# Optimization experiments

Measured on AMD Instinct MI355X. Metric: run time of the kernel, lower is better.

Reference implementation:

```python
import jax, jax.numpy as jnp
import numpy as np

B, N, C = 512, 512, 96  # N = D*H*W with D=H=W=8


def _conv3d(x, w, b, groups=1):
    # x: [B, C, D, H, W], w: [O, I/groups, kd, kh, kw]
    y = jax.lax.conv_general_dilated(
        x, w, window_strides=(1, 1, 1), padding='SAME',
        dimension_numbers=('NCDHW', 'OIDHW', 'NCDHW'),
        feature_group_count=groups)
    return y + b[None, :, None, None, None]


def setup_inputs() -> dict:
    key = jax.random.key(0)
    ks = jax.random.split(key, 8)
    s1 = 0.1   # keep pre-softmax logits in a sane range
    sd = 0.2
    inp = {
        'x': jax.random.normal(ks[0], (B, N, C), jnp.float32),
        'wq1': jax.random.normal(ks[1], (C, C, 1, 1, 1), jnp.float32) * s1,
        'bq1': jnp.zeros((C,), jnp.float32),
        'wk1': jax.random.normal(ks[2], (C, C, 1, 1, 1), jnp.float32) * s1,
        'bk1': jnp.zeros((C,), jnp.float32),
        'wv1': jax.random.normal(ks[3], (C, C, 1, 1, 1), jnp.float32) * s1,
        'bv1': jnp.zeros((C,), jnp.float32),
        'wqd': jax.random.normal(ks[4], (C, 1, 3, 3, 3), jnp.float32) * sd,
        'bqd': jnp.zeros((C,), jnp.float32),
        'wkd': jax.random.normal(ks[5], (C, 1, 3, 3, 3), jnp.float32) * sd,
        'bkd': jnp.zeros((C,), jnp.float32),
        'wvd': jax.random.normal(ks[6], (C, 1, 3, 3, 3), jnp.float32) * sd,
        'bvd': jnp.zeros((C,), jnp.float32),
    }
    return inp


def reference(x, wq1, bq1, wk1, bk1, wv1, bv1, wqd, bqd, wkd, bkd, wvd, bvd):
    b, n, c = x.shape
    d = int(round(n ** (1.0 / 3.0)))
    # [B, N, C] -> [B, C, D, H, W]
    x5 = x.reshape(b, d, d, d, c).transpose(0, 4, 1, 2, 3)
    q = _conv3d(_conv3d(x5, wq1, bq1), wqd, bqd, groups=c)
    k = _conv3d(_conv3d(x5, wk1, bk1), wkd, bkd, groups=c)
    v = _conv3d(_conv3d(x5, wv1, bv1), wvd, bvd, groups=c)
    # [B, C, D, H, W] -> [B, N, C]
    q = q.transpose(0, 2, 3, 4, 1).reshape(b, n, c)
    k = k.transpose(0, 2, 3, 4, 1).reshape(b, n, c)
    v = v.transpose(0, 2, 3, 4, 1).reshape(b, n, c)
    attn = jnp.einsum('bnc,bmc->bnm', q, k) / jnp.sqrt(jnp.float32(c))
    attn = jax.nn.softmax(attn, axis=-1)
    out = jnp.einsum('bnm,bmc->bnc', attn, v)
    return out
```

## Files before the change

### kernel.cpp

```cpp
#include <hip/hip_runtime.h>
#include <math.h>

typedef _Float16 f16;
typedef _Float16 f16x2 __attribute__((ext_vector_type(2)));
typedef _Float16 f16x8 __attribute__((ext_vector_type(8)));
typedef __fp16 fp16x2 __attribute__((ext_vector_type(2)));
typedef float f32x4 __attribute__((ext_vector_type(4)));

union F2U { f16x2 h; fp16x2 p; unsigned u; };
union U2H { uint2 q; f16x2 h[2]; f16 f[4]; };
union U4H { uint4 q; f16x2 h[4]; f16 f[8]; };

__device__ __forceinline__ f16x2 uAsH(unsigned u) { F2U c; c.u = u; return c.h; }
__device__ __forceinline__ unsigned hAsU(f16x2 h) { F2U c; c.h = h; return c.u; }
__device__ __forceinline__ unsigned pAsU(fp16x2 p) { F2U c; c.p = p; return c.u; }

constexpr size_t PL = (size_t)512 * 512 * 96;

__global__ __launch_bounds__(1024, 4) void k12_fused(
    const float* __restrict__ x,
    const float* __restrict__ wq1, const float* __restrict__ bq1,
    const float* __restrict__ wk1, const float* __restrict__ bk1,
    const float* __restrict__ wv1, const float* __restrict__ bv1,
    const float* __restrict__ wqd, const float* __restrict__ bqd,
    const float* __restrict__ wkd, const float* __restrict__ bkd,
    const float* __restrict__ wvd, const float* __restrict__ bvd,
    f16* __restrict__ qo, f16* __restrict__ ko, f16* __restrict__ vo)
{
    __shared__ __align__(16) char sm[137600];
    f16* Xsh = (f16*)sm;
    f16* Wsh = (f16*)(sm + 106496);
    unsigned* wdx = (unsigned*)(sm + 126464);
    float* bl1 = (float*)(sm + 136832);
    float* bld = (float*)(sm + 137216);

    const int tid = threadIdx.x;
    const int b = blockIdx.x;
    const int which = blockIdx.y;
    const int wv_ = tid >> 6, lane = tid & 63, lr = lane & 15, lk = lane >> 4;

    const float* w1 = (which == 0) ? wq1 : ((which == 1) ? wk1 : wv1);
    const float* b1 = (which == 0) ? bq1 : ((which == 1) ? bk1 : bv1);
    const float* wd = (which == 0) ? wqd : ((which == 1) ? wkd : wvd);
    const float* bd = (which == 0) ? bqd : ((which == 1) ? bkd : bvd);

    const float* xb = x + (size_t)b * 512 * 96;
    #pragma unroll
    for (int it = 0; it < 12; ++it) {
        int i = (tid + it * 1024) * 4;
        float4 v4 = *(const float4*)(xb + i);
        int r = i / 96, c = i % 96;
        f16x2 h01 = { (f16)v4.x, (f16)v4.y };
        f16x2 h23 = { (f16)v4.z, (f16)v4.w };
        uint2 st; st.x = hAsU(h01); st.y = hAsU(h23);
        *(uint2*)(Xsh + r * 104 + c) = st;
    }
    #pragma unroll
    for (int it = 0; it < 3; ++it) {
        int i = (tid + it * 1024) * 4;
        if (i < 9216) {
            float4 v4 = *(const float4*)(w1 + i);
            int co = i / 96, ci = i % 96;
            f16x2 h01 = { (f16)v4.x, (f16)v4.y };
            f16x2 h23 = { (f16)v4.z, (f16)v4.w };
            uint2 st; st.x = hAsU(h01); st.y = hAsU(h23);
            *(uint2*)(Wsh + co * 104 + ci) = st;
        }
    }
    if (which < 2) {
        for (int ii = tid; ii < 2592; ii += 1024) {
            int c = ii / 27, t2 = ii % 27;
            ((f16*)wdx)[t2 * 96 + c] = (f16)wd[ii];
        }
    } else {
        for (int ii = tid; ii < 2592; ii += 1024) {
            int c = ii / 27, t2 = ii % 27;
            f16 hh = (f16)wd[ii];
            f16x2 hp = { hh, hh };
            wdx[c * 27 + t2] = hAsU(hp);
        }
    }
    if (tid < 96) { bl1[tid] = b1[tid]; bld[tid] = bd[tid]; }
    __syncthreads();

    f32x4 acc[2][6];
    #pragma unroll
    for (int pg = 0; pg < 2; ++pg)
        #pragma unroll
        for (int cg = 0; cg < 6; ++cg) acc[pg][cg] = f32x4{0.f, 0.f, 0.f, 0.f};

    if (which < 2) {
        #pragma unroll
        for (int ks = 0; ks < 3; ++ks) {
            f16x8 bfr[6];
            #pragma unroll
            for (int cg = 0; cg < 6; ++cg)
                bfr[cg] = *(const f16x8*)(Wsh + (cg * 16 + lr) * 104 + ks * 32 + lk * 8);
            #pragma unroll
            for (int pg = 0; pg < 2; ++pg) {
                f16x8 a = *(const f16x8*)(Xsh + (wv_ * 32 + pg * 16 + lr) * 104 + ks * 32 + lk * 8);
                #pragma unroll
                for (int cg = 0; cg < 6; ++cg)
                    acc[pg][cg] = __builtin_amdgcn_mfma_f32_16x16x32_f16(bfr[cg], a, acc[pg][cg], 0, 0, 0);
            }
        }
    } else {
        #pragma unroll
        for (int ks = 0; ks < 3; ++ks) {
            f16x8 bfr[6];
            #pragma unroll
            for (int cg = 0; cg < 6; ++cg)
                bfr[cg] = *(const f16x8*)(Wsh + (cg * 16 + lr) * 104 + ks * 32 + lk * 8);
            #pragma unroll
            for (int pg = 0; pg < 2; ++pg) {
                f16x8 a = *(const f16x8*)(Xsh + (wv_ * 32 + pg * 16 + lr) * 104 + ks * 32 + lk * 8);
                #pragma unroll
                for (int cg = 0; cg < 6; ++cg)
                    acc[pg][cg] = __builtin_amdgcn_mfma_f32_16x16x32_f16(a, bfr[cg], acc[pg][cg], 0, 0, 0);
            }
        }
    }
    __syncthreads();

    if (which < 2) {
        #pragma unroll
        for (int pg = 0; pg < 2; ++pg) {
            #pragma unroll
            for (int cg = 0; cg < 6; ++cg) {
                float4 bv4 = *(const float4*)&bl1[cg * 16 + lk * 4];
                int pos = wv_ * 32 + pg * 16 + lr;
                f16x2 h01 = { (f16)(acc[pg][cg][0] + bv4.x), (f16)(acc[pg][cg][1] + bv4.y) };
                f16x2 h23 = { (f16)(acc[pg][cg][2] + bv4.z), (f16)(acc[pg][cg][3] + bv4.w) };
                uint2 st; st.x = hAsU(h01); st.y = hAsU(h23);
                *(uint2*)(Xsh + pos * 104 + cg * 16 + lk * 4) = st;
            }
        }
    } else {
        #pragma unroll
        for (int pg = 0; pg < 2; ++pg) {
            #pragma unroll
            for (int cg = 0; cg < 6; ++cg) {
                float bv = bl1[cg * 16 + lr];
                int ch = cg * 16 + lr;
                int pos = wv_ * 32 + pg * 16 + lk * 4;
                f16x2 h01 = { (f16)(acc[pg][cg][0] + bv), (f16)(acc[pg][cg][1] + bv) };
                f16x2 h23 = { (f16)(acc[pg][cg][2] + bv), (f16)(acc[pg][cg][3] + bv) };
                uint2 st; st.x = hAsU(h01); st.y = hAsU(h23);
                *(uint2*)(Xsh + ch * 520 + pos) = st;
            }
        }
    }
    __syncthreads();

    if (which < 2) {
        f16* slab = Xsh;
        unsigned* wdh = wdx;
        f16* outb = ((which == 0) ? qo : ko) + (size_t)b * 512 * 96;
        #pragma unroll
        for (int half = 0; half < 2; ++half) {
            if (half == 1 && tid >= 512) break;
            const int u = half * 1024 + tid;
            const int r = u / 24;
            const int g4 = u - r * 24;
            const int dd = r >> 3, hh = r & 7;
            const int col = g4 * 4;
            float mo[8][4];
            {
                float4 b0 = *(const float4*)&bld[col];
                #pragma unroll
                for (int w = 0; w < 8; ++w) {
                    mo[w][0] = b0.x; mo[w][1] = b0.y; mo[w][2] = b0.z; mo[w][3] = b0.w;
                }
            }
            #pragma unroll
            for (int kd = 0; kd < 3; ++kd) {
                const int d2 = dd + kd - 1;
                const bool vd = (unsigned)d2 < 8u;
                f16x2 pa[8][2];
                #pragma unroll
                for (int w = 0; w < 8; ++w) {
                    pa[w][0] = f16x2{0, 0}; pa[w][1] = f16x2{0, 0};
                }
                #pragma unroll
                for (int kh = 0; kh < 3; ++kh) {
                    const int h2 = hh + kh - 1;
                    const unsigned vm = (vd && ((unsigned)h2 < 8u)) ? 0xFFFFFFFFu : 0u;
                    const int base = (vm ? (d2 * 64 + h2 * 8) : 0) * 104 + col;
                    U2H in[8];
                    #pragma unroll
                    for (int w2 = 0; w2 < 8; ++w2)
                        in[w2].q = *(const uint2*)(slab + base + w2 * 104);
                    const int t0 = (kd * 3 + kh) * 3;
                    f16x2 wt0[2], wt1[2], wt2[2];
                    #pragma unroll
                    for (int p = 0; p < 2; ++p) {
                        wt0[p] = uAsH(wdh[(t0 + 0) * 48 + g4 * 2 + p] & vm);
                        wt1[p] = uAsH(wdh[(t0 + 1) * 48 + g4 * 2 + p] & vm);
                        wt2[p] = uAsH(wdh[(t0 + 2) * 48 + g4 * 2 + p] & vm);
                    }
                    #pragma unroll
                    for (int w = 0; w < 8; ++w) {
                        #pragma unroll
                        for (int p = 0; p < 2; ++p) {
                            f16x2 s = pa[w][p];
                            s = in[w].h[p] * wt1[p] + s;
                            if (w > 0) s = in[w - 1].h[p] * wt0[p] + s;
                            if (w < 7) s = in[w + 1].h[p] * wt2[p] + s;
                            pa[w][p] = s;
                        }
                    }
                }
                #pragma unroll
                for (int w = 0; w < 8; ++w)
                    #pragma unroll
                    for (int p = 0; p < 2; ++p) {
                        mo[w][2 * p]     += (float)pa[w][p].x;
                        mo[w][2 * p + 1] += (float)pa[w][p].y;
                    }
            }
            #pragma unroll
            for (int w = 0; w < 8; ++w) {
                f16x2 h0 = { (f16)mo[w][0], (f16)mo[w][1] };
                f16x2 h1 = { (f16)mo[w][2], (f16)mo[w][3] };
                uint2 st; st.x = hAsU(h0); st.y = hAsU(h1);
                *(uint2*)(outb + (size_t)(r * 8 + w) * 96 + col) = st;
            }
        }
    } else {
        f16* slab = Xsh;
        unsigned* wdp = wdx;
        f16* outb = vo + (size_t)b * 96 * 512;
        #pragma unroll
        for (int j = 0; j < 6; ++j) {
            int u = tid + j * 1024;
            int c = u >> 6, dh = u & 63;
            int dd = dh >> 3, hh2 = dh & 7;
            f16x2 A0[4], A1[4], A2[4];
            #pragma unroll
            for (int p = 0; p < 4; ++p) {
                A0[p] = f16x2{0, 0}; A1[p] = f16x2{0, 0}; A2[p] = f16x2{0, 0};
            }
            #pragma unroll
            for (int kd = 0; kd < 3; ++kd) {
                int d2 = dd + kd - 1;
                unsigned vd_ = ((unsigned)d2 < 8u) ? 0xFFFFFFFFu : 0u;
                #pragma unroll
                for (int kh = 0; kh < 3; ++kh) {
                    int h2 = hh2 + kh - 1;
                    unsigned vm = ((((unsigned)h2 < 8u) ? 0xFFFFFFFFu : 0u) & vd_);
                    int rowoff = vm ? ((d2 * 8 + h2) * 8) : 0;
                    uint4 rw = *(const uint4*)(slab + c * 520 + rowoff);
                    unsigned r0 = rw.x, r1 = rw.y, r2 = rw.z, r3 = rw.w;
                    unsigned ms0 = r0 << 16;
                    unsigned ms1 = (r1 << 16) | (r0 >> 16);
                    unsigned ms2 = (r2 << 16) | (r1 >> 16);
                    unsigned ms3 = (r3 << 16) | (r2 >> 16);
                    unsigned ms4 = r3 >> 16;
                    int t0 = kd * 9 + kh * 3;
                    f16x2 w0 = uAsH(wdp[c * 27 + t0]     & vm);
                    f16x2 w1 = uAsH(wdp[c * 27 + t0 + 1] & vm);
                    f16x2 w2 = uAsH(wdp[c * 27 + t0 + 2] & vm);
                    f16x2* acc2 = (kd == 0) ? A0 : ((kd == 1) ? A1 : A2);
                    acc2[0] = uAsH(ms0) * w0 + acc2[0];
                    acc2[1] = uAsH(ms1) * w0 + acc2[1];
                    acc2[2] = uAsH(ms2) * w0 + acc2[2];
                    acc2[3] = uAsH(ms3) * w0 + acc2[3];
                    acc2[0] = uAsH(r0) * w1 + acc2[0];
                    acc2[1] = uAsH(r1) * w1 + acc2[1];
                    acc2[2] = uAsH(r2) * w1 + acc2[2];
                    acc2[3] = uAsH(r3) * w1 + acc2[3];
                    acc2[0] = uAsH(ms1) * w2 + acc2[0];
                    acc2[1] = uAsH(ms2) * w2 + acc2[1];
                    acc2[2] = uAsH(ms3) * w2 + acc2[2];
                    acc2[3] = uAsH(ms4) * w2 + acc2[3];
                }
            }
            float bv = bld[c];
            unsigned ow[4];
            #pragma unroll
            for (int p = 0; p < 4; ++p) {
                float lo = (float)A0[p].x + (float)A1[p].x + (float)A2[p].x + bv;
                float hi = (float)A0[p].y + (float)A1[p].y + (float)A2[p].y + bv;
                f16x2 hp = { (f16)lo, (f16)hi };
                ow[p] = hAsU(hp);
            }
            *(uint4*)(outb + c * 512 + dh * 8) = make_uint4(ow[0], ow[1], ow[2], ow[3]);
        }
    }
}

__global__ __launch_bounds__(512) void k3_attn(
    const f16* __restrict__ qF, const f16* __restrict__ kF, const f16* __restrict__ vF,
    float* __restrict__ outp)
{
    __shared__ __align__(16) f16 Ksh[512 * 104];
    __shared__ __align__(16) f16 Psh[8 * 1152];

    const int tid = threadIdx.x;
    const int b = blockIdx.x;
    const int wv_ = tid >> 6, lane = tid & 63, lr = lane & 15, lk = lane >> 4;

    const f16* qg = qF + ((size_t)b * 512 + wv_ * 64) * 96;
    const f16* kg = kF + (size_t)b * 512 * 96;
    const f16* vg = vF + (size_t)b * 96 * 512;

    const float scl = 0.14724447f;

    #pragma unroll
    for (int it = 0; it < 12; ++it) {
        int i = tid * 8 + it * 4096;
        int r = i / 96, c = i % 96;
        *(uint4*)(Ksh + r * 104 + c) = *(const uint4*)(kg + i);
    }
    __syncthreads();

    float sum_p[4] = {0.f, 0.f, 0.f, 0.f};
    f32x4 accO[4][6];
    #pragma unroll
    for (int qg2 = 0; qg2 < 4; ++qg2)
        #pragma unroll
        for (int cg = 0; cg < 6; ++cg) accO[qg2][cg] = f32x4{0.f, 0.f, 0.f, 0.f};

    f16* psw = Psh + wv_ * 1152;
    uint2* psw2 = (uint2*)psw;

    for (int t = 0; t < 8; ++t) {
        f16x8 kf[3][4];
        #pragma unroll
        for (int ks3 = 0; ks3 < 3; ++ks3)
            #pragma unroll
            for (int f = 0; f < 4; ++f)
                kf[ks3][f] = *(const f16x8*)(Ksh + (t * 64 + f * 16 + lr) * 104 + ks3 * 32 + lk * 8);
        f16x8 vb[2][6];
        #pragma unroll
        for (int ks2 = 0; ks2 < 2; ++ks2)
            #pragma unroll
            for (int cg = 0; cg < 6; ++cg)
                vb[ks2][cg] = *(const f16x8*)(vg + (size_t)(cg * 16 + lr) * 512
                                                 + t * 64 + ks2 * 32 + lk * 8);
        #pragma unroll
        for (int qg2 = 0; qg2 < 4; ++qg2) {
            f16x8 qf3[3];
            #pragma unroll
            for (int ks3 = 0; ks3 < 3; ++ks3)
                qf3[ks3] = *(const f16x8*)(qg + (qg2 * 16 + lr) * 96 + ks3 * 32 + lk * 8);
            f32x4 sa[4];
            #pragma unroll
            for (int f = 0; f < 4; ++f) sa[f] = f32x4{0.f, 0.f, 0.f, 0.f};
            #pragma unroll
            for (int ks3 = 0; ks3 < 3; ++ks3)
                #pragma unroll
                for (int f = 0; f < 4; ++f)
                    sa[f] = __builtin_amdgcn_mfma_f32_16x16x32_f16(kf[ks3][f], qf3[ks3], sa[f], 0, 0, 0);
            #pragma unroll
            for (int f = 0; f < 4; ++f) {
                float e0 = __builtin_amdgcn_exp2f(sa[f][0] * scl);
                float e1 = __builtin_amdgcn_exp2f(sa[f][1] * scl);
                float e2 = __builtin_amdgcn_exp2f(sa[f][2] * scl);
                float e3 = __builtin_amdgcn_exp2f(sa[f][3] * scl);
                sum_p[qg2] += (e0 + e1) + (e2 + e3);
                uint2 pk;
                pk.x = pAsU(__builtin_amdgcn_cvt_pkrtz(e0, e1));
                pk.y = pAsU(__builtin_amdgcn_cvt_pkrtz(e2, e3));
                psw2[lr * 18 + f * 4 + lk] = pk;
            }
            #pragma unroll
            for (int ks2 = 0; ks2 < 2; ++ks2) {
                f16x8 pb = *(const f16x8*)(psw + lr * 72 + ks2 * 32 + lk * 8);
                #pragma unroll
                for (int cg = 0; cg < 6; ++cg)
                    accO[qg2][cg] = __builtin_amdgcn_mfma_f32_16x16x32_f16(
                        vb[ks2][cg], pb, accO[qg2][cg], 0, 0, 0);
            }
        }
    }
    #pragma unroll
    for (int qg2 = 0; qg2 < 4; ++qg2) {
        sum_p[qg2] += __shfl_xor(sum_p[qg2], 16);
        sum_p[qg2] += __shfl_xor(sum_p[qg2], 32);
    }

    #pragma unroll
    for (int qg2 = 0; qg2 < 4; ++qg2) {
        const float inv = 1.0f / sum_p[qg2];
        float* og = outp + ((size_t)b * 512 + wv_ * 64 + qg2 * 16 + lr) * 96;
        #pragma unroll
        for (int cg = 0; cg < 6; ++cg) {
            float4 o4 = make_float4(accO[qg2][cg][0] * inv, accO[qg2][cg][1] * inv,
                                    accO[qg2][cg][2] * inv, accO[qg2][cg][3] * inv);
            *(float4*)(og + cg * 16 + lk * 4) = o4;
        }
    }
}

extern "C" void kernel_launch(void* const* d_in, const int* in_sizes, int n_in,
                              void* d_out, int out_size, void* d_ws, size_t ws_size,
                              hipStream_t stream) {
    const float* x   = (const float*)d_in[0];
    const float* wq1 = (const float*)d_in[1];
    const float* bq1 = (const float*)d_in[2];
    const float* wk1 = (const float*)d_in[3];
    const float* bk1 = (const float*)d_in[4];
    const float* wv1 = (const float*)d_in[5];
    const float* bv1 = (const float*)d_in[6];
    const float* wqd = (const float*)d_in[7];
    const float* bqd = (const float*)d_in[8];
    const float* wkd = (const float*)d_in[9];
    const float* bkd = (const float*)d_in[10];
    const float* wvd = (const float*)d_in[11];
    const float* bvd = (const float*)d_in[12];

    f16* ws = (f16*)d_ws;
    f16* q = ws;
    f16* k = ws + PL;
    f16* v = ws + 2 * PL;

    k12_fused<<<dim3(512, 3), 1024, 0, stream>>>(x, wq1, bq1, wk1, bk1, wv1, bv1,
                                                 wqd, bqd, wkd, bkd, wvd, bvd, q, k, v);
    k3_attn<<<512, 512, 0, stream>>>(q, k, v, (float*)d_out);
}
```

Before: 246.2 us.

## Split fused conv kernel over channel halves and read x directly into MFMA fragments

The fused 1x1+depthwise conv kernel is now launched with a third grid dimension that splits the 96 output channels into two halves of 48. Blocks shrink from 1024 to 512 threads and shared memory from about 137KB to about 74KB, which should allow more resident blocks and give more parallelism. The x tile is no longer staged in shared memory. Each wave loads fp32 rows from global memory and converts them into f16 MFMA fragments in registers. The trade-off is that each x row is read from global memory twice, once per channel half.

```diff
diff --git a/kernel.cpp b/kernel.cpp
--- a/kernel.cpp
+++ b/kernel.cpp
@@ -10,14 +10,24 @@
 union F2U { f16x2 h; fp16x2 p; unsigned u; };
 union U2H { uint2 q; f16x2 h[2]; f16 f[4]; };
 union U4H { uint4 q; f16x2 h[4]; f16 f[8]; };
+union V8H { f16x8 v; f16x2 h[4]; f16 f[8]; };
 
 __device__ __forceinline__ f16x2 uAsH(unsigned u) { F2U c; c.u = u; return c.h; }
 __device__ __forceinline__ unsigned hAsU(f16x2 h) { F2U c; c.h = h; return c.u; }
 __device__ __forceinline__ unsigned pAsU(fp16x2 p) { F2U c; c.p = p; return c.u; }
 
+__device__ __forceinline__ f16x8 ld8cvt(const float* p) {
+    float4 a = *(const float4*)p;
+    float4 b = *(const float4*)(p + 4);
+    V8H r;
+    r.f[0] = (f16)a.x; r.f[1] = (f16)a.y; r.f[2] = (f16)a.z; r.f[3] = (f16)a.w;
+    r.f[4] = (f16)b.x; r.f[5] = (f16)b.y; r.f[6] = (f16)b.z; r.f[7] = (f16)b.w;
+    return r.v;
+}
+
 constexpr size_t PL = (size_t)512 * 512 * 96;
 
-__global__ __launch_bounds__(1024, 4) void k12_fused(
+__global__ __launch_bounds__(512) void k12_fused(
     const float* __restrict__ x,
     const float* __restrict__ wq1, const float* __restrict__ bq1,
     const float* __restrict__ wk1, const float* __restrict__ bk1,
@@ -27,141 +37,90 @@
     const float* __restrict__ wvd, const float* __restrict__ bvd,
     f16* __restrict__ qo, f16* __restrict__ ko, f16* __restrict__ vo)
 {
-    __shared__ __align__(16) char sm[137600];
-    f16* Xsh = (f16*)sm;
-    f16* Wsh = (f16*)(sm + 106496);
-    unsigned* wdx = (unsigned*)(sm + 126464);
-    float* bl1 = (float*)(sm + 136832);
-    float* bld = (float*)(sm + 137216);
+    __shared__ __align__(16) char sm[74400];
 
     const int tid = threadIdx.x;
     const int b = blockIdx.x;
     const int which = blockIdx.y;
+    const int chalf = blockIdx.z;
+    const int ch0 = chalf * 48;
     const int wv_ = tid >> 6, lane = tid & 63, lr = lane & 15, lk = lane >> 4;
 
     const float* w1 = (which == 0) ? wq1 : ((which == 1) ? wk1 : wv1);
     const float* b1 = (which == 0) ? bq1 : ((which == 1) ? bk1 : bv1);
     const float* wd = (which == 0) ? wqd : ((which == 1) ? wkd : wvd);
     const float* bd = (which == 0) ? bqd : ((which == 1) ? bkd : bvd);
-
     const float* xb = x + (size_t)b * 512 * 96;
-    #pragma unroll
-    for (int it = 0; it < 12; ++it) {
-        int i = (tid + it * 1024) * 4;
-        float4 v4 = *(const float4*)(xb + i);
-        int r = i / 96, c = i % 96;
-        f16x2 h01 = { (f16)v4.x, (f16)v4.y };
-        f16x2 h23 = { (f16)v4.z, (f16)v4.w };
-        uint2 st; st.x = hAsU(h01); st.y = hAsU(h23);
-        *(uint2*)(Xsh + r * 104 + c) = st;
-    }
-    #pragma unroll
-    for (int it = 0; it < 3; ++it) {
-        int i = (tid + it * 1024) * 4;
-        if (i < 9216) {
-            float4 v4 = *(const float4*)(w1 + i);
-            int co = i / 96, ci = i % 96;
-            f16x2 h01 = { (f16)v4.x, (f16)v4.y };
-            f16x2 h23 = { (f16)v4.z, (f16)v4.w };
-            uint2 st; st.x = hAsU(h01); st.y = hAsU(h23);
-            *(uint2*)(Wsh + co * 104 + ci) = st;
-        }
-    }
+
     if (which < 2) {
-        for (int ii = tid; ii < 2592; ii += 1024) {
-            int c = ii / 27, t2 = ii % 27;
-            ((f16*)wdx)[t2 * 96 + c] = (f16)wd[ii];
-        }
-    } else {
-        for (int ii = tid; ii < 2592; ii += 1024) {
-            int c = ii / 27, t2 = ii % 27;
-            f16 hh = (f16)wd[ii];
-            f16x2 hp = { hh, hh };
-            wdx[c * 27 + t2] = hAsU(hp);
-        }
-    }
-    if (tid < 96) { bl1[tid] = b1[tid]; bld[tid] = bd[tid]; }
-    __syncthreads();
-
-    f32x4 acc[2][6];
-    #pragma unroll
-    for (int pg = 0; pg < 2; ++pg)
-        #pragma unroll
-        for (int cg = 0; cg < 6; ++cg) acc[pg][cg] = f32x4{0.f, 0.f, 0.f, 0.f};
-
-    if (which < 2) {
+        f16*      slab = (f16*)sm;
+        f16*      Wsh  = (f16*)(sm + 61440);
+        unsigned* wdh  = (unsigned*)(sm + 71424);
+        float*    bl1  = (float*)(sm + 74016);
+        float*    bld  = (float*)(sm + 74208);
+
+        #pragma unroll
+        for (int it = 0; it < 3; ++it) {
+            int g = tid + it * 512;
+            if (g < 1152) {
+                int i = g * 4;
+                int co = i / 96, ci = i % 96;
+                float4 v4 = *(const float4*)(w1 + (size_t)(ch0 + co) * 96 + ci);
+                f16x2 h01 = { (f16)v4.x, (f16)v4.y };
+                f16x2 h23 = { (f16)v4.z, (f16)v4.w };
+                uint2 st; st.x = hAsU(h01); st.y = hAsU(h23);
+                *(uint2*)(Wsh + co * 104 + ci) = st;
+            }
+        }
+        for (int ii = tid; ii < 1296; ii += 512) {
+            int lc = ii / 27, t2 = ii % 27;
+            ((f16*)wdh)[t2 * 48 + lc] = (f16)wd[(ch0 + lc) * 27 + t2];
+        }
+        if (tid < 48) { bl1[tid] = b1[ch0 + tid]; bld[tid] = bd[ch0 + tid]; }
+        __syncthreads();
+
+        f32x4 acc[4][3];
+        #pragma unroll
+        for (int pg = 0; pg < 4; ++pg)
+            #pragma unroll
+            for (int cg = 0; cg < 3; ++cg) acc[pg][cg] = f32x4{0.f, 0.f, 0.f, 0.f};
         #pragma unroll
         for (int ks = 0; ks < 3; ++ks) {
-            f16x8 bfr[6];
-            #pragma unroll
-            for (int cg = 0; cg < 6; ++cg)
+            f16x8 bfr[3];
+            #pragma unroll
+            for (int cg = 0; cg < 3; ++cg)
                 bfr[cg] = *(const f16x8*)(Wsh + (cg * 16 + lr) * 104 + ks * 32 + lk * 8);
             #pragma unroll
-            for (int pg = 0; pg < 2; ++pg) {
-                f16x8 a = *(const f16x8*)(Xsh + (wv_ * 32 + pg * 16 + lr) * 104 + ks * 32 + lk * 8);
-                #pragma unroll
-                for (int cg = 0; cg < 6; ++cg)
+            for (int pg = 0; pg < 4; ++pg) {
+                f16x8 a = ld8cvt(xb + (size_t)(wv_ * 64 + pg * 16 + lr) * 96 + ks * 32 + lk * 8);
+                #pragma unroll
+                for (int cg = 0; cg < 3; ++cg)
                     acc[pg][cg] = __builtin_amdgcn_mfma_f32_16x16x32_f16(bfr[cg], a, acc[pg][cg], 0, 0, 0);
             }
         }
-    } else {
-        #pragma unroll
-        for (int ks = 0; ks < 3; ++ks) {
-            f16x8 bfr[6];
-            #pragma unroll
-            for (int cg = 0; cg < 6; ++cg)
-                bfr[cg] = *(const f16x8*)(Wsh + (cg * 16 + lr) * 104 + ks * 32 + lk * 8);
-            #pragma unroll
-            for (int pg = 0; pg < 2; ++pg) {
-                f16x8 a = *(const f16x8*)(Xsh + (wv_ * 32 + pg * 16 + lr) * 104 + ks * 32 + lk * 8);
-                #pragma unroll
-                for (int cg = 0; cg < 6; ++cg)
-                    acc[pg][cg] = __builtin_amdgcn_mfma_f32_16x16x32_f16(a, bfr[cg], acc[pg][cg], 0, 0, 0);
-            }
-        }
-    }
-    __syncthreads();
-
-    if (which < 2) {
-        #pragma unroll
-        for (int pg = 0; pg < 2; ++pg) {
-            #pragma unroll
-            for (int cg = 0; cg < 6; ++cg) {
+        __syncthreads();
+
+        #pragma unroll
+        for (int pg = 0; pg < 4; ++pg) {
+            int pos = wv_ * 64 + pg * 16 + lr;
+            #pragma unroll
+            for (int cg = 0; cg < 3; ++cg) {
                 float4 bv4 = *(const float4*)&bl1[cg * 16 + lk * 4];
-                int pos = wv_ * 32 + pg * 16 + lr;
                 f16x2 h01 = { (f16)(acc[pg][cg][0] + bv4.x), (f16)(acc[pg][cg][1] + bv4.y) };
                 f16x2 h23 = { (f16)(acc[pg][cg][2] + bv4.z), (f16)(acc[pg][cg][3] + bv4.w) };
                 uint2 st; st.x = hAsU(h01); st.y = hAsU(h23);
-                *(uint2*)(Xsh + pos * 104 + cg * 16 + lk * 4) = st;
-            }
-        }
-    } else {
-        #pragma unroll
-        for (int pg = 0; pg < 2; ++pg) {
-            #pragma unroll
-            for (int cg = 0; cg < 6; ++cg) {
-                float bv = bl1[cg * 16 + lr];
-                int ch = cg * 16 + lr;
-                int pos = wv_ * 32 + pg * 16 + lk * 4;
-                f16x2 h01 = { (f16)(acc[pg][cg][0] + bv), (f16)(acc[pg][cg][1] + bv) };
-                f16x2 h23 = { (f16)(acc[pg][cg][2] + bv), (f16)(acc[pg][cg][3] + bv) };
-                uint2 st; st.x = hAsU(h01); st.y = hAsU(h23);
-                *(uint2*)(Xsh + ch * 520 + pos) = st;
-            }
-        }
-    }
-    __syncthreads();
-
-    if (which < 2) {
-        f16* slab = Xsh;
-        unsigned* wdh = wdx;
+                *(uint2*)(slab + pos * 60 + cg * 16 + lk * 4) = st;
+            }
+        }
+        __syncthreads();
+
         f16* outb = ((which == 0) ? qo : ko) + (size_t)b * 512 * 96;
         #pragma unroll
         for (int half = 0; half < 2; ++half) {
-            if (half == 1 && tid >= 512) break;
-            const int u = half * 1024 + tid;
-            const int r = u / 24;
-            const int g4 = u - r * 24;
+            if (half == 1 && tid >= 256) break;
+            const int u = half * 512 + tid;
+            const int r = u / 12;
+            const int g4 = u - r * 12;
             const int dd = r >> 3, hh = r & 7;
             const int col = g4 * 4;
             float mo[8][4];
@@ -185,18 +144,18 @@
                 for (int kh = 0; kh < 3; ++kh) {
                     const int h2 = hh + kh - 1;
                     const unsigned vm = (vd && ((unsigned)h2 < 8u)) ? 0xFFFFFFFFu : 0u;
-                    const int base = (vm ? (d2 * 64 + h2 * 8) : 0) * 104 + col;
+                    const int base = (vm ? (d2 * 64 + h2 * 8) : 0) * 60 + col;
                     U2H in[8];
                     #pragma unroll
                     for (int w2 = 0; w2 < 8; ++w2)
-                        in[w2].q = *(const uint2*)(slab + base + w2 * 104);
+                        in[w2].q = *(const uint2*)(slab + base + w2 * 60);
                     const int t0 = (kd * 3 + kh) * 3;
                     f16x2 wt0[2], wt1[2], wt2[2];
                     #pragma unroll
                     for (int p = 0; p < 2; ++p) {
-                        wt0[p] = uAsH(wdh[(t0 + 0) * 48 + g4 * 2 + p] & vm);
-                        wt1[p] = uAsH(wdh[(t0 + 1) * 48 + g4 * 2 + p] & vm);
-                        wt2[p] = uAsH(wdh[(t0 + 2) * 48 + g4 * 2 + p] & vm);
+                        wt0[p] = uAsH(wdh[(t0 + 0) * 24 + g4 * 2 + p] & vm);
+                        wt1[p] = uAsH(wdh[(t0 + 1) * 24 + g4 * 2 + p] & vm);
+                        wt2[p] = uAsH(wdh[(t0 + 2) * 24 + g4 * 2 + p] & vm);
                     }
                     #pragma unroll
                     for (int w = 0; w < 8; ++w) {
@@ -223,16 +182,78 @@
                 f16x2 h0 = { (f16)mo[w][0], (f16)mo[w][1] };
                 f16x2 h1 = { (f16)mo[w][2], (f16)mo[w][3] };
                 uint2 st; st.x = hAsU(h0); st.y = hAsU(h1);
-                *(uint2*)(outb + (size_t)(r * 8 + w) * 96 + col) = st;
+                *(uint2*)(outb + (size_t)(r * 8 + w) * 96 + ch0 + col) = st;
             }
         }
     } else {
-        f16* slab = Xsh;
-        unsigned* wdp = wdx;
+        f16*      Vsh = (f16*)sm;
+        f16*      Wsh = (f16*)(sm + 49920);
+        unsigned* wdp = (unsigned*)(sm + 59904);
+        float*    bl1 = (float*)(sm + 65088);
+        float*    bld = (float*)(sm + 65280);
+
+        #pragma unroll
+        for (int it = 0; it < 3; ++it) {
+            int g = tid + it * 512;
+            if (g < 1152) {
+                int i = g * 4;
+                int co = i / 96, ci = i % 96;
+                float4 v4 = *(const float4*)(w1 + (size_t)(ch0 + co) * 96 + ci);
+                f16x2 h01 = { (f16)v4.x, (f16)v4.y };
+                f16x2 h23 = { (f16)v4.z, (f16)v4.w };
+                uint2 st; st.x = hAsU(h01); st.y = hAsU(h23);
+                *(uint2*)(Wsh + co * 104 + ci) = st;
+            }
+        }
+        for (int ii = tid; ii < 1296; ii += 512) {
+            int lc = ii / 27, t2 = ii % 27;
+            f16 hh = (f16)wd[(ch0 + lc) * 27 + t2];
+            f16x2 hp = { hh, hh };
+            wdp[lc * 27 + t2] = hAsU(hp);
+        }
+        if (tid < 48) { bl1[tid] = b1[ch0 + tid]; bld[tid] = bd[ch0 + tid]; }
+        __syncthreads();
+
+        f32x4 acc[4][3];
+        #pragma unroll
+        for (int pg = 0; pg < 4; ++pg)
+            #pragma unroll
+            for (int cg = 0; cg < 3; ++cg) acc[pg][cg] = f32x4{0.f, 0.f, 0.f, 0.f};
+        #pragma unroll
+        for (int ks = 0; ks < 3; ++ks) {
+            f16x8 bfr[3];
+            #pragma unroll
+            for (int cg = 0; cg < 3; ++cg)
+                bfr[cg] = *(const f16x8*)(Wsh + (cg * 16 + lr) * 104 + ks * 32 + lk * 8);
+            #pragma unroll
+            for (int pg = 0; pg < 4; ++pg) {
+                f16x8 a = ld8cvt(xb + (size_t)(wv_ * 64 + pg * 16 + lr) * 96 + ks * 32 + lk * 8);
+                #pragma unroll
+                for (int cg = 0; cg < 3; ++cg)
+                    acc[pg][cg] = __builtin_amdgcn_mfma_f32_16x16x32_f16(a, bfr[cg], acc[pg][cg], 0, 0, 0);
+            }
+        }
+        __syncthreads();
+
+        #pragma unroll
+        for (int pg = 0; pg < 4; ++pg) {
+            int pos = wv_ * 64 + pg * 16 + lk * 4;
+            #pragma unroll
+            for (int cg = 0; cg < 3; ++cg) {
+                float bv = bl1[cg * 16 + lr];
+                int lc = cg * 16 + lr;
+                f16x2 h01 = { (f16)(acc[pg][cg][0] + bv), (f16)(acc[pg][cg][1] + bv) };
+                f16x2 h23 = { (f16)(acc[pg][cg][2] + bv), (f16)(acc[pg][cg][3] + bv) };
+                uint2 st; st.x = hAsU(h01); st.y = hAsU(h23);
+                *(uint2*)(Vsh + lc * 520 + pos) = st;
+            }
+        }
+        __syncthreads();
+
         f16* outb = vo + (size_t)b * 96 * 512;
         #pragma unroll
         for (int j = 0; j < 6; ++j) {
-            int u = tid + j * 1024;
+            int u = tid + j * 512;
             int c = u >> 6, dh = u & 63;
             int dd = dh >> 3, hh2 = dh & 7;
             f16x2 A0[4], A1[4], A2[4];
@@ -249,7 +270,7 @@
                     int h2 = hh2 + kh - 1;
                     unsigned vm = ((((unsigned)h2 < 8u) ? 0xFFFFFFFFu : 0u) & vd_);
                     int rowoff = vm ? ((d2 * 8 + h2) * 8) : 0;
-                    uint4 rw = *(const uint4*)(slab + c * 520 + rowoff);
+                    uint4 rw = *(const uint4*)(Vsh + c * 520 + rowoff);
                     unsigned r0 = rw.x, r1 = rw.y, r2 = rw.z, r3 = rw.w;
                     unsigned ms0 = r0 << 16;
                     unsigned ms1 = (r1 << 16) | (r0 >> 16);
@@ -284,7 +305,7 @@
                 f16x2 hp = { (f16)lo, (f16)hi };
                 ow[p] = hAsU(hp);
             }
-            *(uint4*)(outb + c * 512 + dh * 8) = make_uint4(ow[0], ow[1], ow[2], ow[3]);
+            *(uint4*)(outb + (size_t)(ch0 + c) * 512 + dh * 8) = make_uint4(ow[0], ow[1], ow[2], ow[3]);
         }
     }
 }
@@ -415,7 +436,7 @@
     f16* k = ws + PL;
     f16* v = ws + 2 * PL;
 
-    k12_fused<<<dim3(512, 3), 1024, 0, stream>>>(x, wq1, bq1, wk1, bk1, wv1, bv1,
-                                                 wqd, bqd, wkd, bkd, wvd, bvd, q, k, v);
+    k12_fused<<<dim3(512, 3, 2), 512, 0, stream>>>(x, wq1, bq1, wk1, bk1, wv1, bv1,
+                                                   wqd, bqd, wkd, bkd, wvd, bvd, q, k, v);
     k3_attn<<<512, 512, 0, stream>>>(q, k, v, (float*)d_out);
 }
```

Measured after the change: 258.6 us. +5.0%, slower.
